# Performance work log

Measured on AMD Instinct MI355X. Metric: run time of the kernel, lower is better.

Reference implementation:

```python
import jax, jax.numpy as jnp
import numpy as np

ALPHA = 0.2  # LeakyReLU negative slope
NEG_INF = -9e15


def setup_inputs() -> dict:
    key = jax.random.key(0)
    k1, k2, k3, k4 = jax.random.split(key, 4)
    B, N, F_in, F_out = 8, 2048, 256, 128
    h = jax.random.normal(k1, (B, N, F_in), dtype=jnp.float32)
    adj = jax.random.randint(k2, (B, N, N), 0, 2, dtype=jnp.int32)
    # xavier_uniform with gain=1.414
    def xavier(k, shape, gain=1.414):
        fan_in, fan_out = shape[0], shape[1]
        limit = gain * np.sqrt(6.0 / (fan_in + fan_out))
        return jax.random.uniform(k, shape, jnp.float32, -limit, limit)
    W = xavier(k3, (F_in, F_out))
    a = xavier(k4, (2 * F_out, 1))
    return {"h": h, "adj": adj, "W": W, "a": a}


def reference(h, adj, W, a):
    # h: [B,N,F_in], adj: [B,N,N], W: [F_in,F_out], a: [2*F_out,1]
    Wh = jnp.einsum('bnf,fe->bne', h, W)  # [B,N,E]
    E = Wh.shape[-1]
    a_src, a_dst = a[:E, 0], a[E:, 0]
    # e[b,i,j] = leakyrelu(Wh[b,i].a_src + Wh[b,j].a_dst)  (additive decomposition
    # of a @ concat(Wh_i, Wh_j) -- same math, no [B,N,N,2E] intermediate)
    s_src = Wh @ a_src  # [B,N]
    s_dst = Wh @ a_dst  # [B,N]
    e = jax.nn.leaky_relu(s_src[:, :, None] + s_dst[:, None, :], negative_slope=ALPHA)
    e = jnp.where(adj > 0, e, NEG_INF)
    attention = jax.nn.softmax(e, axis=2)  # [B,N,N]
    # dropout p=0.0 / eval mode -> identity
    h_prime = jnp.einsum('bij,bje->bie', attention, Wh)
    return jax.nn.elu(h_prime)  # concat=True
```

## Files before the change

kernel.cpp:

```cpp
#include <hip/hip_runtime.h>
#include <hip/hip_bf16.h>

#define GAT_ALPHA 0.2f
#define LOG2E 1.4426950408889634f

typedef float f32x4 __attribute__((ext_vector_type(4)));
typedef int   i32x4 __attribute__((ext_vector_type(4)));
typedef short bf16x8 __attribute__((ext_vector_type(8)));

static constexpr int Nn  = 2048;
static constexpr int FIN = 256;
static constexpr int FO  = 128;

static __device__ __forceinline__ unsigned short f2bf(float x) {
    __hip_bfloat16 h = __float2bfloat16(x);
    return __builtin_bit_cast(unsigned short, h);
}
static __device__ __forceinline__ float bf2f(unsigned short u) {
    unsigned int v = ((unsigned int)u) << 16;
    return __builtin_bit_cast(float, v);
}

__global__ __launch_bounds__(256) void gat_prep(
        const float* __restrict__ W, const float* __restrict__ a,
        float* __restrict__ wa, unsigned int* __restrict__ md_key)
{
    __shared__ float pr[32][8];
    __shared__ float pd[32][8];
    const int t = threadIdx.x;
    const int kl = t >> 3, seg = t & 7;
    const int k = blockIdx.x * 32 + kl;
    float ps = 0.f, pv = 0.f;
    const float* wr = W + (size_t)k * FO + seg * 16;
    #pragma unroll
    for (int f = 0; f < 16; f += 4) {
        f32x4 wv = *(const f32x4*)(wr + f);
        f32x4 as = *(const f32x4*)(a + seg * 16 + f);
        f32x4 ad = *(const f32x4*)(a + FO + seg * 16 + f);
        ps += wv[0]*as[0] + wv[1]*as[1] + wv[2]*as[2] + wv[3]*as[3];
        pv += wv[0]*ad[0] + wv[1]*ad[1] + wv[2]*ad[2] + wv[3]*ad[3];
    }
    pr[kl][seg] = ps; pd[kl][seg] = pv;
    __syncthreads();
    if (t < 32) {
        float s = 0.f, d = 0.f;
        #pragma unroll
        for (int j = 0; j < 8; ++j) { s += pr[t][j]; d += pd[t][j]; }
        wa[blockIdx.x * 32 + t]       = s;
        wa[256 + blockIdx.x * 32 + t] = d;
    }
    if (blockIdx.x == 0 && t < 8) md_key[t] = 0u;
}

__global__ __launch_bounds__(256) void gat_pack(
        const int* __restrict__ adj, unsigned int* __restrict__ mask)
{
    const int t = threadIdx.x, lane = t & 63, w = t >> 6;
    const size_t ibase = ((size_t)blockIdx.x * 4 + w) * 2048;
    const int* src = adj + ibase + lane;
    unsigned int myword = 0;
    #pragma unroll
    for (int c = 0; c < 32; ++c) {
        int v = src[(size_t)c * 64];
        unsigned long long m = __ballot(v > 0);
        if (lane == 2 * c)     myword = (unsigned int)m;
        if (lane == 2 * c + 1) myword = (unsigned int)(m >> 32);
    }
    mask[ibase / 32 + lane] = myword;
}

__global__ __launch_bounds__(256) void gat_wh(
        const float* __restrict__ h, const float* __restrict__ W,
        const float* __restrict__ wa, unsigned short* __restrict__ Wp,
        float* __restrict__ s_src, float* __restrict__ s_dst,
        unsigned int* __restrict__ md_key)
{
    __shared__ unsigned short WT[FO][264];
    __shared__ float wal[512];
    __shared__ float sred[64][4][2];
    __shared__ float red64[64];
    const int t  = threadIdx.x;
    const int b  = blockIdx.x & 7;
    const int n0 = (blockIdx.x >> 3) << 6;

    if (t < 128) *(f32x4*)&wal[t * 4] = *(const f32x4*)&wa[t * 4];
    #pragma unroll
    for (int c = 0; c < 32; ++c) {
        int flat = c * 1024 + t * 4;
        int k = flat >> 7, f = flat & 127;
        f32x4 wv = *(const f32x4*)&W[flat];
        WT[f + 0][k] = f2bf(wv[0]);
        WT[f + 1][k] = f2bf(wv[1]);
        WT[f + 2][k] = f2bf(wv[2]);
        WT[f + 3][k] = f2bf(wv[3]);
    }
    __syncthreads();

    {
        const int row = t >> 2, seg = t & 3;
        const float* hp  = h + ((size_t)(b * Nn + n0 + row)) * FIN + seg * 64;
        const float* was = &wal[seg * 64];
        const float* wad = &wal[256 + seg * 64];
        float ps = 0.f, pv = 0.f;
        #pragma unroll
        for (int j = 0; j < 64; j += 4) {
            f32x4 hv = *(const f32x4*)(hp + j);
            f32x4 sv = *(const f32x4*)(was + j);
            f32x4 dv = *(const f32x4*)(wad + j);
            ps += hv[0]*sv[0] + hv[1]*sv[1] + hv[2]*sv[2] + hv[3]*sv[3];
            pv += hv[0]*dv[0] + hv[1]*dv[1] + hv[2]*dv[2] + hv[3]*dv[3];
        }
        sred[row][seg][0] = ps;
        sred[row][seg][1] = pv;
    }
    __syncthreads();
    if (t < 64) {
        float s = sred[t][0][0] + sred[t][1][0] + sred[t][2][0] + sred[t][3][0];
        float d = sred[t][0][1] + sred[t][1][1] + sred[t][2][1] + sred[t][3][1];
        s_src[b * Nn + n0 + t] = s;
        s_dst[b * Nn + n0 + t] = d;
        red64[t] = d;
    }
    __syncthreads();
    if (t < 16) red64[t] = fmaxf(fmaxf(red64[t], red64[t + 16]),
                                 fmaxf(red64[t + 32], red64[t + 48]));
    __syncthreads();
    if (t == 0) {
        float m = red64[0];
        #pragma unroll
        for (int j = 1; j < 16; ++j) m = fmaxf(m, red64[j]);
        unsigned int bits = __builtin_bit_cast(unsigned int, m);
        unsigned int key  = (bits & 0x80000000u) ? ~bits : (bits | 0x80000000u);
        atomicMax(md_key + b, key);
    }

    const int w = t >> 6, lane = t & 63, n16 = lane & 15, quad = lane >> 4;
    const float* ha = h + ((size_t)(b * Nn + n0 + w * 16 + n16)) * FIN + quad * 8;
    f32x4 acc[8] = {};
    #pragma unroll
    for (int ks = 0; ks < 8; ++ks) {
        f32x4 h0 = *(const f32x4*)(ha + ks * 32);
        f32x4 h1 = *(const f32x4*)(ha + ks * 32 + 4);
        bf16x8 af;
        af[0] = (short)f2bf(h0[0]); af[1] = (short)f2bf(h0[1]);
        af[2] = (short)f2bf(h0[2]); af[3] = (short)f2bf(h0[3]);
        af[4] = (short)f2bf(h1[0]); af[5] = (short)f2bf(h1[1]);
        af[6] = (short)f2bf(h1[2]); af[7] = (short)f2bf(h1[3]);
        #pragma unroll
        for (int nt = 0; nt < 8; ++nt) {
            bf16x8 bfr = *(const bf16x8*)&WT[nt * 16 + n16][ks * 32 + quad * 8];
            acc[nt] = __builtin_amdgcn_mfma_f32_16x16x32_bf16(af, bfr, acc[nt], 0, 0, 0);
        }
    }
    {
        const int v      = (n0 >> 5) + (w >> 1);
        const int quad_p = ((w & 1) << 1) + (quad >> 1);
        const int eoff   = (quad & 1) << 2;
        #pragma unroll
        for (int nt = 0; nt < 8; ++nt) {
            ushort4 pk;
            pk.x = f2bf(acc[nt][0]); pk.y = f2bf(acc[nt][1]);
            pk.z = f2bf(acc[nt][2]); pk.w = f2bf(acc[nt][3]);
            size_t idx = ((((size_t)(b << 6) + v) * 8 + nt) * 64 + quad_p * 16 + n16) * 8 + eoff;
            *(ushort4*)&Wp[idx] = pk;
        }
    }
}

__global__ __launch_bounds__(512, 1) void gat_attn(
        const unsigned int* __restrict__ mask, const unsigned short* __restrict__ Wp,
        const float* __restrict__ s_src, const float* __restrict__ s_dst,
        const unsigned int* __restrict__ md_key, float* __restrict__ out)
{
    constexpr int AS = 132;
    constexpr int MS = 65;
    __shared__ __align__(16) float smem_f[2 * 64 * AS];
    __shared__ __align__(16) unsigned int mlds[64 * MS];
    __shared__ __align__(16) float dlds[Nn];
    __shared__ float l_red[64];
    unsigned short* ldsw = (unsigned short*)smem_f;

    const int t = threadIdx.x, w = t >> 6, lane = t & 63;
    const int n16 = lane & 15, quad = lane >> 4;
    const int rg = w & 1, jwin = w >> 1;
    const int b  = blockIdx.x & 7;
    const int i0 = (blockIdx.x >> 3) << 6;

    if (t < 64) l_red[t] = 0.f;

    const unsigned short* wsrc = Wp + ((size_t)b << 18);

    f32x4 g0[4], gA[4], gB[4];
    #pragma unroll
    for (int p = 0; p < 4; ++p) g0[p] = *(const f32x4*)(wsrc + p * 4096 + t * 8);
    #pragma unroll
    for (int p = 0; p < 4; ++p) gA[p] = *(const f32x4*)(wsrc + 16384 + p * 4096 + t * 8);
    i32x4 m0, m1;
    {
        const unsigned int* msrc = mask + ((size_t)(b * Nn + i0)) * 64 + t * 8;
        m0 = *(const i32x4*)(msrc);
        m1 = *(const i32x4*)(msrc + 4);
    }
    f32x4 dv = *(const f32x4*)(s_dst + b * Nn + t * 4);

    const unsigned int key = md_key[b];
    const unsigned int mb_ = (key & 0x80000000u) ? (key ^ 0x80000000u) : ~key;
    const float mdb = __builtin_bit_cast(float, mb_);
    const int r0 = i0 + rg * 32 + n16;
    const float ssr0 = s_src[b * Nn + r0];
    const float ssr1 = s_src[b * Nn + r0 + 16];
    const float tm0 = ssr0 + mdb, tm1 = ssr1 + mdb;
    const float mi0 = fmaxf(tm0, GAT_ALPHA * tm0) * LOG2E;
    const float mi1 = fmaxf(tm1, GAT_ALPHA * tm1) * LOG2E;
    const float sL0 = ssr0 * LOG2E, sL1 = ssr1 * LOG2E;
    const int jw = (jwin << 5) + (quad << 3);
    const int mrow0 = (rg * 32 + n16) * MS;
    const int mrow1 = mrow0 + 16 * MS;

    #pragma unroll
    for (int p = 0; p < 4; ++p) *(f32x4*)&ldsw[p * 4096 + t * 8] = g0[p];
    {
        const int r = t >> 3, c8 = (t & 7) * 8;
        *(i32x4*)&mlds[r * MS + c8]     = m0;
        *(i32x4*)&mlds[r * MS + c8 + 4] = m1;
    }
    *(f32x4*)&dlds[t * 4] = dv;

    f32x4 acc[2][8] = {};
    float ls0 = 0.f, ls1 = 0.f;
    __syncthreads();

#define GAT_TILE(S, CUR, GP, GN)                                                \
    {                                                                           \
        const int s_ = (S);                                                     \
        const int j0 = s_ << 7;                                                 \
           \
        if (s_ < 14) {                                                          \
            const unsigned short* src = wsrc + (size_t)(s_ + 2) * 16384;        \
            _Pragma("unroll")                                                   \
            for (int p = 0; p < 4; ++p)                                         \
                GN[p] = *(const f32x4*)(src + p * 4096 + t * 8);                \
        }                                                                       \
        const unsigned int mw0 = mlds[mrow0 + (s_ << 2) + jwin];                \
        const unsigned int mw1 = mlds[mrow1 + (s_ << 2) + jwin];                \
        const unsigned int mb0 = (mw0 >> (quad << 3)) & 0xffu;                  \
        const unsigned int mb1 = (mw1 >> (quad << 3)) & 0xffu;                  \
        f32x4 d0 = *(const f32x4*)&dlds[j0 + jw];                               \
        f32x4 d1 = *(const f32x4*)&dlds[j0 + jw + 4];                           \
        bf16x8 af0, af1;                                                        \
        _Pragma("unroll")                                                       \
        for (int j = 0; j < 4; ++j) {                                           \
            {   float u  = __builtin_fmaf(d0[j], LOG2E, sL0);                   \
                float lr = fmaxf(u, GAT_ALPHA * u);                             \
                float e  = __builtin_amdgcn_exp2f(lr - mi0);                    \
                e = ((mb0 >> j) & 1u) ? e : 0.f;                                \
                unsigned short us = f2bf(e);                                    \
                ls0 += bf2f(us); af0[j] = (short)us; }                          \
            {   float u  = __builtin_fmaf(d1[j], LOG2E, sL0);                   \
                float lr = fmaxf(u, GAT_ALPHA * u);                             \
                float e  = __builtin_amdgcn_exp2f(lr - mi0);                    \
                e = ((mb0 >> (4 + j)) & 1u) ? e : 0.f;                          \
                unsigned short us = f2bf(e);                                    \
                ls0 += bf2f(us); af0[4 + j] = (short)us; }                      \
            {   float u  = __builtin_fmaf(d0[j], LOG2E, sL1);                   \
                float lr = fmaxf(u, GAT_ALPHA * u);                             \
                float e  = __builtin_amdgcn_exp2f(lr - mi1);                    \
                e = ((mb1 >> j) & 1u) ? e : 0.f;                                \
                unsigned short us = f2bf(e);                                    \
                ls1 += bf2f(us); af1[j] = (short)us; }                          \
            {   float u  = __builtin_fmaf(d1[j], LOG2E, sL1);                   \
                float lr = fmaxf(u, GAT_ALPHA * u);                             \
                float e  = __builtin_amdgcn_exp2f(lr - mi1);                    \
                e = ((mb1 >> (4 + j)) & 1u) ? e : 0.f;                          \
                unsigned short us = f2bf(e);                                    \
                ls1 += bf2f(us); af1[4 + j] = (short)us; }                      \
        }                                                                       \
        const unsigned short* bbase = &ldsw[(CUR) * 16384 + (jwin << 12) + (lane << 3)]; \
        _Pragma("unroll")                                                       \
        for (int nt = 0; nt < 8; ++nt) {                                        \
            bf16x8 bfr = *(const bf16x8*)(bbase + (nt << 9));                   \
            acc[0][nt] = __builtin_amdgcn_mfma_f32_16x16x32_bf16(af0, bfr, acc[0][nt], 0, 0, 0); \
            acc[1][nt] = __builtin_amdgcn_mfma_f32_16x16x32_bf16(af1, bfr, acc[1][nt], 0, 0, 0); \
        }                                                                       \
              \
        if (s_ < 15) {                                                          \
            _Pragma("unroll")                                                   \
            for (int p = 0; p < 4; ++p)                                         \
                *(f32x4*)&ldsw[((CUR) ^ 1) * 16384 + p * 4096 + t * 8] = GP[p]; \
        }                                                                       \
        asm volatile("s_waitcnt lgkmcnt(0)" ::: "memory");                      \
        __builtin_amdgcn_s_barrier();                                           \
    }

    for (int s = 0; s < 16; s += 2) {
        GAT_TILE(s,     0, gA, gB)
        GAT_TILE(s + 1, 1, gB, gA)
    }
#undef GAT_TILE

    ls0 += __shfl_xor(ls0, 16); ls0 += __shfl_xor(ls0, 32);
    ls1 += __shfl_xor(ls1, 16); ls1 += __shfl_xor(ls1, 32);
    if (quad == 0) {
        atomicAdd(&l_red[rg * 32 + n16], ls0);
        atomicAdd(&l_red[rg * 32 + 16 + n16], ls1);
    }

    float* slot = smem_f + (size_t)(jwin & 1) * (64 * AS);
    const int rbase = rg * 32;
    if (jwin < 2) {
        #pragma unroll
        for (int ig = 0; ig < 2; ++ig)
            #pragma unroll
            for (int nt = 0; nt < 8; ++nt)
                #pragma unroll
                for (int rr = 0; rr < 4; ++rr)
                    slot[(size_t)(rbase + ig * 16 + quad * 4 + rr) * AS + nt * 16 + n16] = acc[ig][nt][rr];
    }
    __syncthreads();
    if (jwin >= 2) {
        #pragma unroll
        for (int ig = 0; ig < 2; ++ig)
            #pragma unroll
            for (int nt = 0; nt < 8; ++nt)
                #pragma unroll
                for (int rr = 0; rr < 4; ++rr)
                    slot[(size_t)(rbase + ig * 16 + quad * 4 + rr) * AS + nt * 16 + n16] += acc[ig][nt][rr];
    }
    __syncthreads();

    float* ob = out + ((size_t)(b * Nn + i0)) * FO;
    #pragma unroll
    for (int c = 0; c < 4; ++c) {
        int flat = c * 2048 + t * 4;
        int m = flat >> 7, f = flat & 127;
        f32x4 v0 = *(const f32x4*)&smem_f[(size_t)m * AS + f];
        f32x4 v1 = *(const f32x4*)&smem_f[(size_t)(64 + m) * AS + f];
        float l = l_red[m];
        f32x4 o;
        #pragma unroll
        for (int j = 0; j < 4; ++j) {
            float x = (v0[j] + v1[j]) / l;
            o[j] = x > 0.f ? x : expm1f(x);
        }
        *(f32x4*)&ob[(size_t)m * FO + f] = o;
    }
}

extern "C" void kernel_launch(void* const* d_in, const int* in_sizes, int n_in,
                              void* d_out, int out_size, void* d_ws, size_t ws_size,
                              hipStream_t stream)
{
    const float* h   = (const float*)d_in[0];
    const int*   adj = (const int*)d_in[1];
    const float* W   = (const float*)d_in[2];
    const float* a   = (const float*)d_in[3];
    float* out = (float*)d_out;

    char* ws = (char*)d_ws;
    unsigned short* Wp  = (unsigned short*)ws;
    float* s_src        = (float*)(ws + 4194304);
    float* s_dst        = (float*)(ws + 4259840);
    float* wa           = (float*)(ws + 4325376);
    unsigned int* md_key= (unsigned int*)(ws + 4327424);
    unsigned int* mask  = (unsigned int*)(ws + 8388608);

    hipLaunchKernelGGL(gat_prep, dim3(8),    dim3(256), 0, stream, W, a, wa, md_key);
    hipLaunchKernelGGL(gat_wh,   dim3(256),  dim3(256), 0, stream, h, W, wa, Wp, s_src, s_dst, md_key);
    hipLaunchKernelGGL(gat_pack, dim3(4096), dim3(256), 0, stream, adj, mask);
    hipLaunchKernelGGL(gat_attn, dim3(256),  dim3(512), 0, stream, mask, Wp, s_src, s_dst, md_key, out);
}
```

Before: 247.0 us.

## Fuse adjacency bitmask packing into attention kernel with pipelined adj loads

Removes the separate gat_pack kernel and instead has gat_attn read the int32 adjacency directly, ballot-packing it into LDS bitmask words one tile ahead of use. Adjacency loads are double-buffered in registers alongside the Wh tile prefetch. This avoids writing and rereading the packed mask in global memory and saves a kernel launch. The cost is more registers (32 extra ints per thread) and more global traffic inside the attention loop, which may pressure occupancy at 512 threads.

```diff
diff --git a/kernel.cpp b/kernel.cpp
--- a/kernel.cpp
+++ b/kernel.cpp
@@ -50,23 +50,6 @@
         wa[256 + blockIdx.x * 32 + t] = d;
     }
     if (blockIdx.x == 0 && t < 8) md_key[t] = 0u;
-}
-
-__global__ __launch_bounds__(256) void gat_pack(
-        const int* __restrict__ adj, unsigned int* __restrict__ mask)
-{
-    const int t = threadIdx.x, lane = t & 63, w = t >> 6;
-    const size_t ibase = ((size_t)blockIdx.x * 4 + w) * 2048;
-    const int* src = adj + ibase + lane;
-    unsigned int myword = 0;
-    #pragma unroll
-    for (int c = 0; c < 32; ++c) {
-        int v = src[(size_t)c * 64];
-        unsigned long long m = __ballot(v > 0);
-        if (lane == 2 * c)     myword = (unsigned int)m;
-        if (lane == 2 * c + 1) myword = (unsigned int)(m >> 32);
-    }
-    mask[ibase / 32 + lane] = myword;
 }
 
 __global__ __launch_bounds__(256) void gat_wh(
@@ -168,12 +151,12 @@
 }
 
 __global__ __launch_bounds__(512, 1) void gat_attn(
-        const unsigned int* __restrict__ mask, const unsigned short* __restrict__ Wp,
+        const int* __restrict__ adj, const unsigned short* __restrict__ Wp,
         const float* __restrict__ s_src, const float* __restrict__ s_dst,
         const unsigned int* __restrict__ md_key, float* __restrict__ out)
 {
     constexpr int AS = 132;
-    constexpr int MS = 65;
+    constexpr int MS = 68;
     __shared__ __align__(16) float smem_f[2 * 64 * AS];
     __shared__ __align__(16) unsigned int mlds[64 * MS];
     __shared__ __align__(16) float dlds[Nn];
@@ -188,20 +171,24 @@
 
     if (t < 64) l_red[t] = 0.f;
 
+    const int* abase = adj + ((size_t)(b * Nn + i0 + w * 8)) * Nn + lane;
     const unsigned short* wsrc = Wp + ((size_t)b << 18);
 
+    int av0[16], avC[16], avN[16];
+    #pragma unroll
+    for (int k = 0; k < 16; ++k)
+        av0[k] = abase[(size_t)(k >> 1) * Nn + ((k & 1) << 6)];
+    #pragma unroll
+    for (int k = 0; k < 16; ++k)
+        avC[k] = abase[(size_t)(k >> 1) * Nn + 128 + ((k & 1) << 6)];
     f32x4 g0[4], gA[4], gB[4];
     #pragma unroll
-    for (int p = 0; p < 4; ++p) g0[p] = *(const f32x4*)(wsrc + p * 4096 + t * 8);
-    #pragma unroll
-    for (int p = 0; p < 4; ++p) gA[p] = *(const f32x4*)(wsrc + 16384 + p * 4096 + t * 8);
-    i32x4 m0, m1;
-    {
-        const unsigned int* msrc = mask + ((size_t)(b * Nn + i0)) * 64 + t * 8;
-        m0 = *(const i32x4*)(msrc);
-        m1 = *(const i32x4*)(msrc + 4);
-    }
-    f32x4 dv = *(const f32x4*)(s_dst + b * Nn + t * 4);
+    for (int p = 0; p < 4; ++p)
+        g0[p] = *(const f32x4*)(wsrc + p * 4096 + t * 8);
+    #pragma unroll
+    for (int p = 0; p < 4; ++p)
+        gA[p] = *(const f32x4*)(wsrc + 16384 + p * 4096 + t * 8);
+    *(f32x4*)&dlds[t * 4] = *(const f32x4*)(s_dst + b * Nn + t * 4);
 
     const unsigned int key = md_key[b];
     const unsigned int mb_ = (key & 0x80000000u) ? (key ^ 0x80000000u) : ~key;
@@ -218,29 +205,39 @@
     const int mrow1 = mrow0 + 16 * MS;
 
     #pragma unroll
-    for (int p = 0; p < 4; ++p) *(f32x4*)&ldsw[p * 4096 + t * 8] = g0[p];
-    {
-        const int r = t >> 3, c8 = (t & 7) * 8;
-        *(i32x4*)&mlds[r * MS + c8]     = m0;
-        *(i32x4*)&mlds[r * MS + c8 + 4] = m1;
-    }
-    *(f32x4*)&dlds[t * 4] = dv;
+    for (int k = 0; k < 16; ++k) {
+        unsigned long long m = __ballot(av0[k] > 0);
+        const int rr = k >> 1, c = k & 1;
+        if (lane == 0) mlds[(w * 8 + rr) * MS + (c << 1)]     = (unsigned int)m;
+        if (lane == 1) mlds[(w * 8 + rr) * MS + (c << 1) + 1] = (unsigned int)(m >> 32);
+    }
+    #pragma unroll
+    for (int p = 0; p < 4; ++p)
+        *(f32x4*)&ldsw[p * 4096 + t * 8] = g0[p];
 
     f32x4 acc[2][8] = {};
     float ls0 = 0.f, ls1 = 0.f;
     __syncthreads();
 
-#define GAT_TILE(S, CUR, GP, GN)                                                \
+#define GAT_TILE(S, CUR, AVC, AVN, GP, GN)                                      \
     {                                                                           \
         const int s_ = (S);                                                     \
         const int j0 = s_ << 7;                                                 \
-           \
+                    \
+        if (s_ < 14) {                                                          \
+            const int coff = (s_ + 2) << 7;                                     \
+            _Pragma("unroll")                                                   \
+            for (int k = 0; k < 16; ++k)                                        \
+                AVN[k] = abase[(size_t)(k >> 1) * Nn + coff + ((k & 1) << 6)];  \
+        }                                                                       \
+                 \
         if (s_ < 14) {                                                          \
             const unsigned short* src = wsrc + (size_t)(s_ + 2) * 16384;        \
             _Pragma("unroll")                                                   \
             for (int p = 0; p < 4; ++p)                                         \
                 GN[p] = *(const f32x4*)(src + p * 4096 + t * 8);                \
         }                                                                       \
+                                                   \
         const unsigned int mw0 = mlds[mrow0 + (s_ << 2) + jwin];                \
         const unsigned int mw1 = mlds[mrow1 + (s_ << 2) + jwin];                \
         const unsigned int mb0 = (mw0 >> (quad << 3)) & 0xffu;                  \
@@ -282,7 +279,18 @@
             acc[0][nt] = __builtin_amdgcn_mfma_f32_16x16x32_bf16(af0, bfr, acc[0][nt], 0, 0, 0); \
             acc[1][nt] = __builtin_amdgcn_mfma_f32_16x16x32_bf16(af1, bfr, acc[1][nt], 0, 0, 0); \
         }                                                                       \
-              \
+            \
+        if (s_ < 15) {                                                          \
+            _Pragma("unroll")                                                   \
+            for (int k = 0; k < 16; ++k) {                                      \
+                unsigned long long m = __ballot(AVC[k] > 0);                    \
+                const int rr = k >> 1, c = k & 1;                               \
+                const int wd = ((s_ + 1) << 2) + (c << 1);                      \
+                if (lane == 0) mlds[(w * 8 + rr) * MS + wd]     = (unsigned int)m; \
+                if (lane == 1) mlds[(w * 8 + rr) * MS + wd + 1] = (unsigned int)(m >> 32); \
+            }                                                                   \
+        }                                                                       \
+               \
         if (s_ < 15) {                                                          \
             _Pragma("unroll")                                                   \
             for (int p = 0; p < 4; ++p)                                         \
@@ -293,8 +301,8 @@
     }
 
     for (int s = 0; s < 16; s += 2) {
-        GAT_TILE(s,     0, gA, gB)
-        GAT_TILE(s + 1, 1, gB, gA)
+        GAT_TILE(s,     0, avC, avN, gA, gB)
+        GAT_TILE(s + 1, 1, avN, avC, gB, gA)
     }
 #undef GAT_TILE
 
@@ -362,10 +370,8 @@
     float* s_dst        = (float*)(ws + 4259840);
     float* wa           = (float*)(ws + 4325376);
     unsigned int* md_key= (unsigned int*)(ws + 4327424);
-    unsigned int* mask  = (unsigned int*)(ws + 8388608);
-
-    hipLaunchKernelGGL(gat_prep, dim3(8),    dim3(256), 0, stream, W, a, wa, md_key);
-    hipLaunchKernelGGL(gat_wh,   dim3(256),  dim3(256), 0, stream, h, W, wa, Wp, s_src, s_dst, md_key);
-    hipLaunchKernelGGL(gat_pack, dim3(4096), dim3(256), 0, stream, adj, mask);
-    hipLaunchKernelGGL(gat_attn, dim3(256),  dim3(512), 0, stream, mask, Wp, s_src, s_dst, md_key, out);
-}
+
+    hipLaunchKernelGGL(gat_prep, dim3(8),   dim3(256), 0, stream, W, a, wa, md_key);
+    hipLaunchKernelGGL(gat_wh,   dim3(256), dim3(256), 0, stream, h, W, wa, Wp, s_src, s_dst, md_key);
+    hipLaunchKernelGGL(gat_attn, dim3(256), dim3(512), 0, stream, adj, Wp, s_src, s_dst, md_key, out);
+}
```

Result: faster. 236.3 us (-4.4%).
